# Optimization experiments

Hardware: AMD Instinct MI355X
Metric: run time of the kernel (lower is better)

The kernel has to match this reference:

```python
import jax, jax.numpy as jnp
import numpy as np

D = 128            # indexer head dim == fp8 quant group size
ROT = 64           # dims rotated by rope (index_head_dim - rope_head_dim)
LN_EPS = 1e-6
Q_EPS = 1e-4       # eps in sgl_per_token_group_quant_fp8
FP8_MAX = 448.0    # e4m3fn max
NEG = -1e30        # finite -inf stand-in for masking

_Hnp = np.array([[1.0]], dtype=np.float64)
for _ in range(7):
    _Hnp = np.block([[_Hnp, _Hnp], [_Hnp, -_Hnp]])
HAD = jnp.asarray(_Hnp, dtype=jnp.float32)  # 128x128 Sylvester Hadamard


def _hadamard(x):
    # rotate_activation: hadamard_transform(x, scale=d**-0.5), bf16 in/out
    return (x.astype(jnp.float32) @ HAD * (D ** -0.5)).astype(jnp.bfloat16)


def _rope(x, cos, sin):
    # non-interleaved rope on last dim (size ROT), cos/sin have ROT//2 entries
    half = cos.shape[-1]
    x1, x2 = x[..., :half], x[..., half:]
    return jnp.concatenate([x1 * cos - x2 * sin, x2 * cos + x1 * sin], axis=-1)


def _quant_fp8(x):
    # per-128-group fp8 e4m3 quant; here last dim == group size == 128
    xf = x.astype(jnp.float32)
    amax = jnp.max(jnp.abs(xf), axis=-1, keepdims=True)
    scale = jnp.maximum(amax, Q_EPS) / FP8_MAX
    q = (xf / scale).astype(jnp.float8_e4m3fn)
    return q, scale


def setup_inputs() -> dict:
    key = jax.random.key(0)
    ks = jax.random.split(key, 6)
    T, H, HID, QL = 1024, 64, 7168, 1536
    hidden_states = jax.random.normal(ks[0], (T, HID), dtype=jnp.bfloat16)
    q_lora = jax.random.normal(ks[1], (T, QL), dtype=jnp.bfloat16)
    wq_b = (jax.random.normal(ks[2], (QL, H * D), dtype=jnp.float32) * 0.02).astype(jnp.bfloat16)
    wk = (jax.random.normal(ks[3], (HID, D), dtype=jnp.float32) * 0.02).astype(jnp.bfloat16)
    k_norm_w = jnp.ones((D,), dtype=jnp.float32)
    k_norm_b = jnp.zeros((D,), dtype=jnp.float32)
    weights_proj_w = jax.random.normal(ks[4], (HID, H), dtype=jnp.float32) * 0.02
    # realistic rope cos/sin cache: [T, ROT] = cos(32) | sin(32)
    pos = jnp.arange(T, dtype=jnp.float32)[:, None]
    inv_freq = 1.0 / (10000.0 ** (jnp.arange(0, ROT // 2, dtype=jnp.float32) * 2.0 / ROT))
    freqs = pos * inv_freq[None, :]
    cos_sin_cache = jnp.concatenate([jnp.cos(freqs), jnp.sin(freqs)], axis=-1)
    positions = jnp.arange(T, dtype=jnp.int32)
    return {
        "hidden_states": hidden_states, "q_lora": q_lora, "wq_b": wq_b, "wk": wk,
        "k_norm_w": k_norm_w, "k_norm_b": k_norm_b, "weights_proj_w": weights_proj_w,
        "cos_sin_cache": cos_sin_cache, "positions": positions, "topk": 1024,
    }


def reference(hidden_states, q_lora, wq_b, wk, k_norm_w, k_norm_b,
              weights_proj_w, cos_sin_cache, positions, topk):
    T = hidden_states.shape[0]
    H = wq_b.shape[1] // D
    half = ROT // 2
    softmax_scale = D ** -0.5
    weights_scale = H ** -0.5

    # q/k projections (bf16 linears)
    q = (q_lora @ wq_b).reshape(T, H, D)            # [T,H,128] bf16
    k = hidden_states @ wk                           # [T,128] bf16

    # k layernorm in fp32
    kf = k.astype(jnp.float32)
    mu = kf.mean(-1, keepdims=True)
    var = kf.var(-1, keepdims=True)
    k = ((kf - mu) * jax.lax.rsqrt(var + LN_EPS) * k_norm_w + k_norm_b).astype(jnp.bfloat16)

    # rope on first ROT dims (non-interleaved)
    cs = cos_sin_cache[positions]                    # [T,64]
    cos, sin = cs[:, :half], cs[:, half:]
    q_rot = _rope(q[..., :ROT].astype(jnp.float32), cos[:, None, :], sin[:, None, :]).astype(jnp.bfloat16)
    q = jnp.concatenate([q_rot, q[..., ROT:]], axis=-1)
    k_rot = _rope(k[:, :ROT].astype(jnp.float32), cos, sin).astype(jnp.bfloat16)
    k = jnp.concatenate([k_rot, k[:, ROT:]], axis=-1)

    # hadamard rotation
    query = _hadamard(q)                             # [T,H,128]
    key = _hadamard(k)                               # [T,128]

    # fp8 per-group quant (group == head dim)
    q_fp8, q_scale = _quant_fp8(query.reshape(T * H, D))
    q_fp8 = q_fp8.reshape(T, H, D)
    q_scale = q_scale.reshape(T, H)
    k_fp8, k_scale = _quant_fp8(key)                 # [T,128], [T,1]

    # head gate weights: weights_proj(x.float()) * q_scale * softmax_scale * n_heads**-0.5
    weights = (hidden_states.astype(jnp.float32) @ weights_proj_w) * q_scale * (softmax_scale * weights_scale)

    # fp8_mqa_logits: logits[t,j] = sum_h weights[t,h] * relu(q_fp8[t,h] . (k_fp8[j]*k_scale[j]))
    k_deq = k_fp8.astype(jnp.float32) * k_scale
    scores = jax.nn.relu(jnp.einsum('thd,jd->thj', q_fp8.astype(jnp.float32), k_deq))
    logits = jnp.einsum('thj,th->tj', scores, weights)

    # ragged causal validity: ks=0, ke=pos+1
    mask = jnp.arange(T, dtype=jnp.int32)[None, :] <= positions[:, None]
    logits = jnp.where(mask, logits, NEG)

    # fused top-k transform: indices of top-k valid keys, -1 padded
    vals, idx = jax.lax.top_k(logits, topk)
    topk_idx = jnp.where(vals > NEG * 0.5, idx, -1).astype(jnp.int32)
    return topk_idx, logits
```

## Files before the change

### kernel.cpp

```cpp
#include <hip/hip_runtime.h>

typedef unsigned short u16;
typedef unsigned int u32;
typedef unsigned long long u64;
typedef __bf16 bf16x8 __attribute__((ext_vector_type(8)));
typedef float f32x4 __attribute__((ext_vector_type(4)));
typedef unsigned short ushort8 __attribute__((ext_vector_type(8)));
typedef long long ll2 __attribute__((ext_vector_type(2)));
typedef int v4i __attribute__((ext_vector_type(4)));
typedef int v8i __attribute__((ext_vector_type(8)));

#define NEGF (-1e30f)
#define HAD_SCALE 0.08838834764831845f
#define WCONST 0.011048543456039806f
#define SA 64.0f
#define SB 1024.0f
#define DEQ (1.0f / 65536.0f)
#define SCL1 0x7f7f7f7f

__device__ __forceinline__ float b2f(u16 u) {
  union { u32 i; float f; } x; x.i = ((u32)u) << 16; return x.f;
}
__device__ __forceinline__ u16 f2b(float f) {
  u32 u = __float_as_uint(f);
  return (u16)((u + 0x7fffu + ((u >> 16) & 1u)) >> 16);
}
__device__ __forceinline__ float bfr(float f) { return b2f(f2b(f)); }

__device__ __forceinline__ void async_cp16(void* lds, const void* g) {
  __builtin_amdgcn_global_load_lds((__attribute__((address_space(1))) void*)g,
                                   (__attribute__((address_space(3))) void*)lds, 16, 0, 0);
}

__device__ __forceinline__ u32 pk4_fp8(float a, float b, float c, float d) {
  u32 w = (u32)__builtin_amdgcn_cvt_pk_fp8_f32(a, b, 0, false);
  w = (u32)__builtin_amdgcn_cvt_pk_fp8_f32(c, d, (int)w, true);
  return w;
}

__device__ __forceinline__ v8i cat8(v4i lo, v4i hi) {
  return __builtin_shufflevector(lo, hi, 0, 1, 2, 3, 4, 5, 6, 7);
}

__device__ __forceinline__ size_t pk_granule(int r4, int k) {
  return (size_t)((k >> 6) * 1024 + (((k >> 3) & 3) * 16 + r4) * 16 + (((k >> 5) & 1) * 8));
}
__device__ __forceinline__ int pk_u32_idx(int r4, int li) {
  return (li >> 4) * 256 + (((li >> 1) & 3) * 16 + r4) * 4 + ((li >> 3) & 1) * 2 + (li & 1);
}

__device__ __forceinline__ void tr_tile(const void* src, u16* dst, int Nn,
                                        int dpitch, int f32src, int k0, int n0,
                                        u16* tl) {
  int tid = threadIdx.x;
  int kk = tid >> 3, nc = tid & 7;
  u16 v[8];
  if (f32src) {
    const float* s = (const float*)src + (size_t)(k0 + kk) * Nn + n0 + nc * 8;
#pragma unroll
    for (int j = 0; j < 8; ++j) v[j] = f2b(s[j]);
  } else {
    const u16* s = (const u16*)src + (size_t)(k0 + kk) * Nn + n0 + nc * 8;
    ushort8 x = *(const ushort8*)s;
#pragma unroll
    for (int j = 0; j < 8; ++j) v[j] = x[j];
  }
#pragma unroll
  for (int j = 0; j < 8; ++j) tl[(nc * 8 + j) * 56 + kk] = v[j];
  __syncthreads();
  int n = tid >> 2, kc = tid & 3;
  ushort8 o = *(const ushort8*)(tl + n * 56 + kc * 8);
  *(ushort8*)(dst + (size_t)(n0 + n) * dpitch + k0 + kc * 8) = o;
}

__global__ __launch_bounds__(256) void prep_transpose(const u16* __restrict__ wq_b,
                                                      const u16* __restrict__ wk,
                                                      const float* __restrict__ wproj,
                                                      const u16* __restrict__ q_lora,
                                                      unsigned char* __restrict__ wq8,
                                                      unsigned char* __restrict__ aq8,
                                                      u16* __restrict__ BT2) {
  __shared__ u16 tl[64 * 72];
  int b = blockIdx.x, tid = threadIdx.x;
  if (b < 3072) {
    int kt0 = (b % 24) * 64, n0 = (b / 24) * 64;
#pragma unroll
    for (int i = 0; i < 2; ++i) {
      int s = i * 256 + tid;
      int row = s >> 3, c = s & 7;
      ushort8 x = *(const ushort8*)(wq_b + (size_t)(kt0 + row) * 8192 + n0 + c * 8);
#pragma unroll
      for (int j = 0; j < 8; ++j) tl[(c * 8 + j) * 72 + row] = x[j];
    }
    __syncthreads();
    int n = tid >> 2, kc = tid & 3;
    const u16* src = tl + n * 72 + kc * 16;
    u32 w[4];
#pragma unroll
    for (int g = 0; g < 4; ++g)
      w[g] = pk4_fp8(b2f(src[4 * g]) * SB, b2f(src[4 * g + 1]) * SB,
                     b2f(src[4 * g + 2]) * SB, b2f(src[4 * g + 3]) * SB);
    int gn = n0 + n;
    int k1 = kt0 + kc * 16;
    size_t ga = (size_t)(gn >> 4) * 24576 + pk_granule(gn & 15, k1);
    *(u64*)(wq8 + ga) = (u64)w[0] | ((u64)w[1] << 32);
    *(u64*)(wq8 + ga + 256) = (u64)w[2] | ((u64)w[3] << 32);
  } else if (b < 3520) {
    int g = b - 3072;
    tr_tile(wk, BT2, 128, 7168, 0, (g % 224) * 32, (g / 224) * 64, tl);
  } else if (b < 3744) {
    int g = b - 3520;
    tr_tile(wproj, BT2 + (size_t)128 * 7168, 64, 7168, 1, g * 32, 0, tl);
  } else if (b < 3808) {
    int r = 192 + (b - 3744);
    ushort8 z = {0, 0, 0, 0, 0, 0, 0, 0};
    u16* row = BT2 + (size_t)r * 7168;
    for (int i = tid; i < 896; i += 256) *(ushort8*)(row + i * 8) = z;
  } else {
    int mb = b - 3808;
#pragma unroll
    for (int it = 0; it < 6; ++it) {
      int id = it * 256 + tid;
      int c = id >> 4, r = id & 15;
      const u16* src = q_lora + (size_t)(mb * 16 + r) * 1536 + c * 16;
      ushort8 x0 = *(const ushort8*)src;
      ushort8 x1 = *(const ushort8*)(src + 8);
      u32 w0 = pk4_fp8(b2f(x0[0]) * SA, b2f(x0[1]) * SA, b2f(x0[2]) * SA, b2f(x0[3]) * SA);
      u32 w1 = pk4_fp8(b2f(x0[4]) * SA, b2f(x0[5]) * SA, b2f(x0[6]) * SA, b2f(x0[7]) * SA);
      u32 w2 = pk4_fp8(b2f(x1[0]) * SA, b2f(x1[1]) * SA, b2f(x1[2]) * SA, b2f(x1[3]) * SA);
      u32 w3 = pk4_fp8(b2f(x1[4]) * SA, b2f(x1[5]) * SA, b2f(x1[6]) * SA, b2f(x1[7]) * SA);
      size_t ga = (size_t)mb * 24576 + pk_granule(r, c * 16);
      *(u64*)(aq8 + ga) = (u64)w0 | ((u64)w1 << 32);
      *(u64*)(aq8 + ga + 256) = (u64)w2 | ((u64)w3 << 32);
    }
  }
}

__device__ __forceinline__ void planar4(float v0, float v1, float v2, float v3,
                                        int li, float4 c4, float4 s4,
                                        u32* __restrict__ dst_word,
                                        float* __restrict__ dstscale) {
  float p0 = __shfl_xor(v0, 8, 64);
  float p1 = __shfl_xor(v1, 8, 64);
  float p2 = __shfl_xor(v2, 8, 64);
  float p3 = __shfl_xor(v3, 8, 64);
  if (li < 8) {
    v0 = bfr(v0 * c4.x - p0 * s4.x); v1 = bfr(v1 * c4.y - p1 * s4.y);
    v2 = bfr(v2 * c4.z - p2 * s4.z); v3 = bfr(v3 * c4.w - p3 * s4.w);
  } else if (li < 16) {
    v0 = bfr(v0 * c4.x + p0 * s4.x); v1 = bfr(v1 * c4.y + p1 * s4.y);
    v2 = bfr(v2 * c4.z + p2 * s4.z); v3 = bfr(v3 * c4.w + p3 * s4.w);
  }
  { float a = v0 + v1, b = v0 - v1; v0 = a; v1 = b; }
  { float a = v2 + v3, b = v2 - v3; v2 = a; v3 = b; }
  { float a = v0 + v2, b = v0 - v2; v0 = a; v2 = b; }
  { float a = v1 + v3, b = v1 - v3; v1 = a; v3 = b; }
#pragma unroll
  for (int m = 1; m <= 16; m <<= 1) {
    float q0 = __shfl_xor(v0, m, 64), q1 = __shfl_xor(v1, m, 64);
    float q2 = __shfl_xor(v2, m, 64), q3 = __shfl_xor(v3, m, 64);
    if (li & m) { v0 = q0 - v0; v1 = q1 - v1; v2 = q2 - v2; v3 = q3 - v3; }
    else        { v0 += q0;     v1 += q1;     v2 += q2;     v3 += q3; }
  }
  v0 = bfr(v0 * HAD_SCALE); v1 = bfr(v1 * HAD_SCALE);
  v2 = bfr(v2 * HAD_SCALE); v3 = bfr(v3 * HAD_SCALE);
  float am = fmaxf(fmaxf(fabsf(v0), fabsf(v1)), fmaxf(fabsf(v2), fabsf(v3)));
#pragma unroll
  for (int m = 1; m <= 16; m <<= 1) am = fmaxf(am, __shfl_xor(am, m, 64));
  am = fmaxf(am, 1e-4f);
  float scale = am / 448.0f;
  float inv = 1.0f / scale;
  *dst_word = pk4_fp8(v0 * inv, v1 * inv, v2 * inv, v3 * inv);
  if (li == 0) *dstscale = scale;
}

__global__ __launch_bounds__(256) void gemm_merged(const unsigned char* __restrict__ A,
                                                   const unsigned char* __restrict__ B,
                                                   const float* __restrict__ cs,
                                                   const int* __restrict__ positions,
                                                   u32* __restrict__ q_fp8,
                                                   float* __restrict__ q_scale,
                                                   const u16* __restrict__ hidden,
                                                   const u16* __restrict__ BT2,
                                                   float* __restrict__ part) {
  __shared__ unsigned char smem[24576];
  int tid = threadIdx.x, wid = tid >> 6, lane = tid & 63, lo = lane & 15, quad = lane >> 4;

  if (blockIdx.x >= 1024) {
    u16* As = (u16*)smem;
    u16* Bs = (u16*)smem + 4096;
    int flat = blockIdx.x - 1024;
    int z = flat & 7, up = flat >> 3;
    int m0 = (up & 15) * 64, n0 = (up >> 4) * 128;
    int mrow = (wid & 1) * 32, nrow = (wid >> 1) * 64;
    f32x4 zero4 = {0.f, 0.f, 0.f, 0.f};
    f32x4 acc[2][4];
#pragma unroll
    for (int a = 0; a < 2; ++a)
#pragma unroll
      for (int b = 0; b < 4; ++b) acc[a][b] = zero4;
    for (int kb = 0; kb < 896; kb += 64) {
      int k0 = z * 896 + kb;
#pragma unroll
      for (int i = 0; i < 2; ++i) {
        int s = i * 256 + tid;
        int row = s >> 3, c = s & 7, kc = c ^ (row & 7);
        async_cp16(As + (size_t)s * 8, hidden + (size_t)(m0 + row) * 7168 + k0 + kc * 8);
      }
#pragma unroll
      for (int i = 0; i < 4; ++i) {
        int s = i * 256 + tid;
        int row = s >> 3, c = s & 7, kc = c ^ (row & 7);
        async_cp16(Bs + (size_t)s * 8, BT2 + (size_t)(n0 + row) * 7168 + k0 + kc * 8);
      }
      __syncthreads();
#pragma unroll
      for (int ksub = 0; ksub < 2; ++ksub) {
        bf16x8 af[2], bfm[4];
#pragma unroll
        for (int mt = 0; mt < 2; ++mt) {
          int r = mrow + mt * 16 + lo;
          af[mt] = *(const bf16x8*)(As + r * 64 + (((ksub * 4 + quad) ^ (r & 7)) * 8));
        }
#pragma unroll
        for (int nt = 0; nt < 4; ++nt) {
          int r = nrow + nt * 16 + lo;
          bfm[nt] = *(const bf16x8*)(Bs + r * 64 + (((ksub * 4 + quad) ^ (r & 7)) * 8));
        }
#pragma unroll
        for (int mt = 0; mt < 2; ++mt)
#pragma unroll
          for (int nt = 0; nt < 4; ++nt)
            acc[mt][nt] = __builtin_amdgcn_mfma_f32_16x16x32_bf16(af[mt], bfm[nt], acc[mt][nt], 0, 0, 0);
      }
      __syncthreads();
    }
    float* dst = part + (size_t)z * 262144;
#pragma unroll
    for (int mt = 0; mt < 2; ++mt)
#pragma unroll
      for (int nt = 0; nt < 4; ++nt)
#pragma unroll
        for (int r = 0; r < 4; ++r)
          dst[(size_t)(m0 + mrow + mt * 16 + quad * 4 + r) * 256 +
              (n0 + nrow + nt * 16 + lo)] = acc[mt][nt][r];
    return;
  }

  unsigned char* As = smem;
  unsigned char* Bs = smem + 8192;
  int flat = blockIdx.x;
  int xcd = flat & 7, lid = flat >> 3;
  int m0 = (lid & 15) * 64;
  int head = xcd * 8 + (lid >> 4);
  int n0 = head * 128;
  int mb0 = m0 >> 4, nb0 = n0 >> 4;
  int wm = wid & 1, wn = wid >> 1;
  int mrow = wm * 32, nrow = wn * 64;
  f32x4 zero4 = {0.f, 0.f, 0.f, 0.f};
  f32x4 acc[2][4];
#pragma unroll
  for (int a = 0; a < 2; ++a)
#pragma unroll
    for (int b = 0; b < 4; ++b) acc[a][b] = zero4;

  for (int k0 = 0; k0 < 1536; k0 += 128) {
    int pg0 = k0 >> 6;
#pragma unroll
    for (int i = 0; i < 2; ++i) {
      int s = i * 256 + tid;
      int u = s >> 6, l64 = s & 63;
      async_cp16(As + (size_t)s * 16,
                 A + (size_t)(mb0 + (u >> 1)) * 24576 + (size_t)(pg0 + (u & 1)) * 1024 + l64 * 16);
    }
#pragma unroll
    for (int i = 0; i < 4; ++i) {
      int s = i * 256 + tid;
      int u = s >> 6, l64 = s & 63;
      async_cp16(Bs + (size_t)s * 16,
                 B + (size_t)(nb0 + (u >> 1)) * 24576 + (size_t)(pg0 + (u & 1)) * 1024 + l64 * 16);
    }
    __syncthreads();
    v8i av[2], bv[4];
#pragma unroll
    for (int mt = 0; mt < 2; ++mt) {
      v4i l0 = *(const v4i*)(As + ((wm * 2 + mt) * 2 + 0) * 1024 + lane * 16);
      v4i h0 = *(const v4i*)(As + ((wm * 2 + mt) * 2 + 1) * 1024 + lane * 16);
      av[mt] = cat8(l0, h0);
    }
#pragma unroll
    for (int nt = 0; nt < 4; ++nt) {
      v4i l0 = *(const v4i*)(Bs + ((wn * 4 + nt) * 2 + 0) * 1024 + lane * 16);
      v4i h0 = *(const v4i*)(Bs + ((wn * 4 + nt) * 2 + 1) * 1024 + lane * 16);
      bv[nt] = cat8(l0, h0);
    }
#pragma unroll
    for (int mt = 0; mt < 2; ++mt)
#pragma unroll
      for (int nt = 0; nt < 4; ++nt)
        acc[mt][nt] = __builtin_amdgcn_mfma_scale_f32_16x16x128_f8f6f4(
            av[mt], bv[nt], acc[mt][nt], 0, 0, 0, SCL1, 0, SCL1);
    __syncthreads();
  }
  u16* ct = (u16*)smem;
#pragma unroll
  for (int mt = 0; mt < 2; ++mt)
#pragma unroll
    for (int nt = 0; nt < 4; ++nt)
#pragma unroll
      for (int r = 0; r < 4; ++r)
        ct[(mrow + mt * 16 + quad * 4 + r) * 136 + (nrow + nt * 16 + lo)] =
            f2b(acc[mt][nt][r] * DEQ);
  __syncthreads();
  int li = lane & 31, half = lane >> 5;
  int hw = wid * 2 + half;
  int qi = pk_u32_idx(head & 15, li) + (head >> 4) * 512;
#pragma unroll
  for (int i = 0; i < 8; ++i) {
    int r = hw * 8 + i;
    int t = m0 + r;
    u64 raw = *(const u64*)(ct + r * 136 + 4 * li);
    float v0 = b2f((u16)raw), v1 = b2f((u16)(raw >> 16));
    float v2 = b2f((u16)(raw >> 32)), v3 = b2f((u16)(raw >> 48));
    const float* csrow = cs + (size_t)positions[t] * 64;
    float4 c4 = make_float4(1.f, 1.f, 1.f, 1.f), s4 = make_float4(0.f, 0.f, 0.f, 0.f);
    if (li < 16) {
      c4 = *(const float4*)(csrow + 4 * (li & 7));
      s4 = *(const float4*)(csrow + 32 + 4 * (li & 7));
    }
    planar4(v0, v1, v2, v3, li, c4, s4,
            q_fp8 + (size_t)t * 2048 + qi, q_scale + t * 64 + head);
  }
}

__global__ __launch_bounds__(256) void k_epilogue(const float* __restrict__ kpart,
                                                  const float* __restrict__ knw,
                                                  const float* __restrict__ knb,
                                                  const float* __restrict__ cs,
                                                  const int* __restrict__ positions,
                                                  u32* __restrict__ k_fp8,
                                                  float* __restrict__ k_scale,
                                                  float* __restrict__ kaccw) {
  int wid = threadIdx.x >> 6, lane = threadIdx.x & 63;
  int li = lane & 31, half = lane >> 5;
  int t = blockIdx.x * 8 + wid * 2 + half;
  const float* base = kpart + (size_t)t * 256;
  float v0 = 0.f, v1 = 0.f, v2 = 0.f, v3 = 0.f, w0 = 0.f, w1 = 0.f;
#pragma unroll
  for (int z = 0; z < 8; ++z) {
    const float* p = base + (size_t)z * 262144;
    f32x4 kv = *(const f32x4*)(p + 4 * li);
    float2 wv = *(const float2*)(p + 128 + 2 * li);
    v0 += kv.x; v1 += kv.y; v2 += kv.z; v3 += kv.w;
    w0 += wv.x; w1 += wv.y;
  }
  *(float2*)(kaccw + (size_t)t * 64 + 2 * li) = make_float2(w0, w1);
  v0 = bfr(v0); v1 = bfr(v1); v2 = bfr(v2); v3 = bfr(v3);
  float sm = v0 + v1 + v2 + v3;
  float sq = v0 * v0 + v1 * v1 + v2 * v2 + v3 * v3;
#pragma unroll
  for (int m = 1; m <= 16; m <<= 1) {
    sm += __shfl_xor(sm, m, 64);
    sq += __shfl_xor(sq, m, 64);
  }
  float mean = sm * (1.0f / 128.0f);
  float var = sq * (1.0f / 128.0f) - mean * mean;
  float rstd = rsqrtf(var + 1e-6f);
  f32x4 g = *(const f32x4*)(knw + 4 * li);
  f32x4 bb = *(const f32x4*)(knb + 4 * li);
  v0 = bfr((v0 - mean) * rstd * g.x + bb.x);
  v1 = bfr((v1 - mean) * rstd * g.y + bb.y);
  v2 = bfr((v2 - mean) * rstd * g.z + bb.z);
  v3 = bfr((v3 - mean) * rstd * g.w + bb.w);
  const float* csrow = cs + (size_t)positions[t] * 64;
  float4 c4 = make_float4(1.f, 1.f, 1.f, 1.f), s4 = make_float4(0.f, 0.f, 0.f, 0.f);
  if (li < 16) {
    c4 = *(const float4*)(csrow + 4 * (li & 7));
    s4 = *(const float4*)(csrow + 32 + 4 * (li & 7));
  }
  planar4(v0, v1, v2, v3, li, c4, s4,
          k_fp8 + (size_t)(t >> 4) * 512 + pk_u32_idx(t & 15, li), k_scale + t);
}

__global__ __launch_bounds__(256) void scores_kernel(const unsigned char* __restrict__ q_fp8,
                                                     const unsigned char* __restrict__ k_fp8,
                                                     const float* __restrict__ q_scale,
                                                     const float* __restrict__ k_scale,
                                                     const float* __restrict__ kaccw,
                                                     const int* __restrict__ positions,
                                                     float* __restrict__ out) {
  __shared__ unsigned char kt[16384];
  __shared__ float wfinL[256];
  __shared__ float ksL[128];
  int flat = blockIdx.x, tid = threadIdx.x;
  int jt0 = flat >> 8, g = flat & 255;
  int t0 = 4 * g, j0 = 128 * jt0;
  float* logits = out + (size_t)1048576;
#pragma unroll
  for (int e = 0; e < 2; ++e) {
    int ent = e * 256 + tid;
    int tt = t0 + (ent >> 7), j = j0 + (ent & 127);
    out[(size_t)tt * 1024 + j] = (j <= positions[tt]) ? (float)j : -1.0f;
  }
  if (j0 > t0 + 3) {
#pragma unroll
    for (int e = 0; e < 2; ++e) {
      int ent = e * 256 + tid;
      int tt = t0 + (ent >> 7), j = j0 + (ent & 127);
      logits[(size_t)tt * 1024 + j] = NEGF;
    }
    return;
  }
#pragma unroll
  for (int i = 0; i < 4; ++i)
    async_cp16(kt + (size_t)(i * 256 + tid) * 16,
               k_fp8 + (size_t)j0 * 128 + (size_t)(i * 256 + tid) * 16);
  {
    int tl = tid >> 6, h = tid & 63;
    wfinL[tid] = kaccw[(size_t)(t0 + tl) * 64 + h] *
                 q_scale[(size_t)(t0 + tl) * 64 + h] * WCONST;
  }
  if (tid < 128) ksL[tid] = k_scale[j0 + tid];
  int wid = tid >> 6, lane = tid & 63, lo = lane & 15, quad = lane >> 4;
  int t = t0 + wid;
  int pt = positions[t];
  v8i a8[4];
  const unsigned char* qbase = q_fp8 + (size_t)t * 8192;
#pragma unroll
  for (int ht = 0; ht < 4; ++ht) {
    v4i l0 = *(const v4i*)(qbase + ht * 2048 + lane * 16);
    v4i h0 = *(const v4i*)(qbase + ht * 2048 + 1024 + lane * 16);
    a8[ht] = cat8(l0, h0);
  }
  __syncthreads();
  float wf[4][4];
#pragma unroll
  for (int ht = 0; ht < 4; ++ht)
#pragma unroll
    for (int r = 0; r < 4; ++r) wf[ht][r] = wfinL[wid * 64 + ht * 16 + quad * 4 + r];
  f32x4 zero4 = {0.f, 0.f, 0.f, 0.f};
#pragma unroll
  for (int jc = 0; jc < 2; ++jc) {
    f32x4 acc[4][4];
#pragma unroll
    for (int ht = 0; ht < 4; ++ht)
#pragma unroll
      for (int jt = 0; jt < 4; ++jt) acc[ht][jt] = zero4;
    v8i bv[4];
#pragma unroll
    for (int jt = 0; jt < 4; ++jt) {
      v4i l0 = *(const v4i*)(kt + (jc * 4 + jt) * 2048 + lane * 16);
      v4i h0 = *(const v4i*)(kt + (jc * 4 + jt) * 2048 + 1024 + lane * 16);
      bv[jt] = cat8(l0, h0);
    }
#pragma unroll
    for (int ht = 0; ht < 4; ++ht)
#pragma unroll
      for (int jt = 0; jt < 4; ++jt)
        acc[ht][jt] = __builtin_amdgcn_mfma_scale_f32_16x16x128_f8f6f4(
            a8[ht], bv[jt], acc[ht][jt], 0, 0, 0, SCL1, 0, SCL1);
#pragma unroll
    for (int jt = 0; jt < 4; ++jt) {
      float v = 0.f;
#pragma unroll
      for (int ht = 0; ht < 4; ++ht)
#pragma unroll
        for (int r = 0; r < 4; ++r)
          v += fmaxf(acc[ht][jt][r], 0.f) * wf[ht][r];
      v += __shfl_xor(v, 16, 64);
      v += __shfl_xor(v, 32, 64);
      int jloc = jc * 64 + jt * 16 + lo;
      int j = j0 + jloc;
      if (quad == 0)
        logits[(size_t)t * 1024 + j] = (j <= pt) ? v * ksL[jloc] : NEGF;
    }
  }
}

extern "C" void kernel_launch(void* const* d_in, const int* in_sizes, int n_in,
                              void* d_out, int out_size, void* d_ws, size_t ws_size,
                              hipStream_t stream) {
  const u16* hidden = (const u16*)d_in[0];
  const u16* q_lora = (const u16*)d_in[1];
  const u16* wq_b   = (const u16*)d_in[2];
  const u16* wk     = (const u16*)d_in[3];
  const float* knw  = (const float*)d_in[4];
  const float* knb  = (const float*)d_in[5];
  const float* wproj= (const float*)d_in[6];
  const float* cs   = (const float*)d_in[7];
  const int* pos    = (const int*)d_in[8];
  float* out = (float*)d_out;

  char* ws = (char*)d_ws;
  u16* BT2            = (u16*)(ws);
  float* kpart        = (float*)(ws + 3670016);
  float* kaccw        = (float*)(ws + 20447232);
  unsigned char* wq8  = (unsigned char*)(ws + 20709376);
  unsigned char* aq8  = (unsigned char*)(ws + 33292288);
  unsigned char* qf8  = (unsigned char*)(ws + 34865152);
  float* qsc          = (float*)(ws + 43253760);
  unsigned char* kf8  = (unsigned char*)(ws + 43515904);
  float* ksc          = (float*)(ws + 43646976);

  prep_transpose<<<3872, 256, 0, stream>>>(wq_b, wk, wproj, q_lora, wq8, aq8, BT2);

  gemm_merged<<<1280, 256, 0, stream>>>(aq8, wq8, cs, pos, (u32*)qf8, qsc,
                                        hidden, BT2, kpart);
  k_epilogue<<<128, 256, 0, stream>>>(kpart, knw, knb, cs, pos, (u32*)kf8, ksc, kaccw);

  scores_kernel<<<2048, 256, 0, stream>>>(qf8, kf8, qsc, ksc, kaccw, pos, out);

  (void)in_sizes; (void)n_in; (void)out_size; (void)ws_size;
}
```

Measured before the change: 184.3 us.

## Load fp8 GEMM operands directly into registers with prefetch, drop LDS staging

The fp8 q-projection GEMM no longer stages A/B tiles through shared memory with barriers. Each wave loads its pre-swizzled MFMA fragments straight from global memory into registers and prefetches the next k-step while the current MFMAs run. The bf16 weights-proj split-K blocks move to the front of the grid, and shared memory shrinks so more blocks can be resident. The cost is redundant global loads across waves (each A fragment is read by two waves and each B fragment by two), more registers for the double buffers, and reliance on L2 caching.

New measurement: 191.2 us. +3.7%, slower.

```diff
diff --git a/kernel.cpp b/kernel.cpp
--- a/kernel.cpp
+++ b/kernel.cpp
@@ -6,7 +6,6 @@
 typedef __bf16 bf16x8 __attribute__((ext_vector_type(8)));
 typedef float f32x4 __attribute__((ext_vector_type(4)));
 typedef unsigned short ushort8 __attribute__((ext_vector_type(8)));
-typedef long long ll2 __attribute__((ext_vector_type(2)));
 typedef int v4i __attribute__((ext_vector_type(4)));
 typedef int v8i __attribute__((ext_vector_type(8)));
 
@@ -183,13 +182,13 @@
                                                    const u16* __restrict__ hidden,
                                                    const u16* __restrict__ BT2,
                                                    float* __restrict__ part) {
-  __shared__ unsigned char smem[24576];
+  __shared__ unsigned char smem[17408];
   int tid = threadIdx.x, wid = tid >> 6, lane = tid & 63, lo = lane & 15, quad = lane >> 4;
 
-  if (blockIdx.x >= 1024) {
+  if (blockIdx.x < 256) {
     u16* As = (u16*)smem;
     u16* Bs = (u16*)smem + 4096;
-    int flat = blockIdx.x - 1024;
+    int flat = blockIdx.x;
     int z = flat & 7, up = flat >> 3;
     int m0 = (up & 15) * 64, n0 = (up >> 4) * 128;
     int mrow = (wid & 1) * 32, nrow = (wid >> 1) * 64;
@@ -247,9 +246,7 @@
     return;
   }
 
-  unsigned char* As = smem;
-  unsigned char* Bs = smem + 8192;
-  int flat = blockIdx.x;
+  int flat = blockIdx.x - 256;
   int xcd = flat & 7, lid = flat >> 3;
   int m0 = (lid & 15) * 64;
   int head = xcd * 8 + (lid >> 4);
@@ -264,35 +261,28 @@
 #pragma unroll
     for (int b = 0; b < 4; ++b) acc[a][b] = zero4;
 
-  for (int k0 = 0; k0 < 1536; k0 += 128) {
-    int pg0 = k0 >> 6;
-#pragma unroll
-    for (int i = 0; i < 2; ++i) {
-      int s = i * 256 + tid;
-      int u = s >> 6, l64 = s & 63;
-      async_cp16(As + (size_t)s * 16,
-                 A + (size_t)(mb0 + (u >> 1)) * 24576 + (size_t)(pg0 + (u & 1)) * 1024 + l64 * 16);
-    }
-#pragma unroll
-    for (int i = 0; i < 4; ++i) {
-      int s = i * 256 + tid;
-      int u = s >> 6, l64 = s & 63;
-      async_cp16(Bs + (size_t)s * 16,
-                 B + (size_t)(nb0 + (u >> 1)) * 24576 + (size_t)(pg0 + (u & 1)) * 1024 + l64 * 16);
-    }
-    __syncthreads();
-    v8i av[2], bv[4];
-#pragma unroll
-    for (int mt = 0; mt < 2; ++mt) {
-      v4i l0 = *(const v4i*)(As + ((wm * 2 + mt) * 2 + 0) * 1024 + lane * 16);
-      v4i h0 = *(const v4i*)(As + ((wm * 2 + mt) * 2 + 1) * 1024 + lane * 16);
-      av[mt] = cat8(l0, h0);
-    }
-#pragma unroll
-    for (int nt = 0; nt < 4; ++nt) {
-      v4i l0 = *(const v4i*)(Bs + ((wn * 4 + nt) * 2 + 0) * 1024 + lane * 16);
-      v4i h0 = *(const v4i*)(Bs + ((wn * 4 + nt) * 2 + 1) * 1024 + lane * 16);
-      bv[nt] = cat8(l0, h0);
+  const unsigned char* pa = A + (size_t)(mb0 + wm * 2) * 24576 + lane * 16;
+  const unsigned char* pb = B + (size_t)(nb0 + wn * 4) * 24576 + lane * 16;
+  v8i av[2], bv[4], avn[2], bvn[4];
+#pragma unroll
+  for (int mt = 0; mt < 2; ++mt)
+    av[mt] = cat8(*(const v4i*)(pa + (size_t)mt * 24576),
+                  *(const v4i*)(pa + (size_t)mt * 24576 + 1024));
+#pragma unroll
+  for (int nt = 0; nt < 4; ++nt)
+    bv[nt] = cat8(*(const v4i*)(pb + (size_t)nt * 24576),
+                  *(const v4i*)(pb + (size_t)nt * 24576 + 1024));
+  for (int k = 0; k < 12; ++k) {
+    if (k < 11) {
+      size_t ko = (size_t)(k + 1) * 2048;
+#pragma unroll
+      for (int mt = 0; mt < 2; ++mt)
+        avn[mt] = cat8(*(const v4i*)(pa + (size_t)mt * 24576 + ko),
+                       *(const v4i*)(pa + (size_t)mt * 24576 + ko + 1024));
+#pragma unroll
+      for (int nt = 0; nt < 4; ++nt)
+        bvn[nt] = cat8(*(const v4i*)(pb + (size_t)nt * 24576 + ko),
+                       *(const v4i*)(pb + (size_t)nt * 24576 + ko + 1024));
     }
 #pragma unroll
     for (int mt = 0; mt < 2; ++mt)
@@ -300,7 +290,10 @@
       for (int nt = 0; nt < 4; ++nt)
         acc[mt][nt] = __builtin_amdgcn_mfma_scale_f32_16x16x128_f8f6f4(
             av[mt], bv[nt], acc[mt][nt], 0, 0, 0, SCL1, 0, SCL1);
-    __syncthreads();
+#pragma unroll
+    for (int mt = 0; mt < 2; ++mt) av[mt] = avn[mt];
+#pragma unroll
+    for (int nt = 0; nt < 4; ++nt) bv[nt] = bvn[nt];
   }
   u16* ct = (u16*)smem;
 #pragma unroll
```
